# Performance work log

Measured on AMD Instinct MI355X. Metric: run time of the kernel, lower is better.

Reference implementation:

```python
import jax, jax.numpy as jnp
import numpy as np

EPS = 1e-6
K = 20
NUM_OBJECTS = 50
OBJ_FEAT = 256
C_DIM = 128
HIDDEN = 128


def vn_linear(x, W):
    # x: [B, C, 3, ...]; W: [O, C] -> [B, O, 3, ...]
    return jnp.einsum('oc,bc...->bo...', W, x)


def vn_leaky(x, Wdir, slope):
    d = vn_linear(x, Wdir)
    dot = jnp.sum(x * d, axis=2, keepdims=True)
    dsq = jnp.sum(d * d, axis=2, keepdims=True)
    x_neg = x - (dot / (dsq + EPS)) * d
    return slope * x + (1.0 - slope) * jnp.where(dot >= 0, x, x_neg)


def vn_linear_leaky(x, Wfeat, Wdir, slope):
    pf = vn_linear(x, Wfeat)
    d = vn_linear(x, Wdir)
    dot = jnp.sum(pf * d, axis=2, keepdims=True)
    dsq = jnp.sum(d * d, axis=2, keepdims=True)
    p_neg = pf - (dot / (dsq + EPS)) * d
    return slope * pf + (1.0 - slope) * jnp.where(dot >= 0, pf, p_neg)


def resblock(x, fc0, fc1, a0, a1, sc):
    net = vn_linear(vn_leaky(x, a0, 0.0), fc0)
    dx = vn_linear(vn_leaky(net, a1, 0.0), fc1)
    return vn_linear(x, sc) + dx


def get_graph_feature_cross(x, k):
    # x: [B, 3, N] -> edge features [B, 3, 3, N, k]
    inner = -2.0 * jnp.einsum('bdn,bdm->bnm', x, x)
    xx = jnp.sum(x * x, axis=1)                       # [B, N]
    neg_dist = -xx[:, :, None] - inner - xx[:, None, :]  # [B, N, N]
    idx = jax.lax.top_k(neg_dist, k)[1]               # [B, N, k] nearest neighbors
    xt = jnp.transpose(x, (0, 2, 1))                  # [B, N, 3]
    nbr = jax.vmap(lambda pts, ind: pts[ind])(xt, idx)  # [B, N, k, 3]
    ctr = jnp.broadcast_to(xt[:, :, None, :], nbr.shape)
    cross = jnp.cross(nbr, ctr)
    feat = jnp.stack([nbr - ctr, ctr, cross], axis=3)  # [B, N, k, 3, 3]
    return jnp.transpose(feat, (0, 3, 4, 1, 2))


def mlp2(zf, w0, w1, w2):
    h = jax.nn.relu(zf @ w0.T)
    h = jax.nn.relu(h @ w1.T)
    return h @ w2.T


def setup_inputs():
    key = jax.random.key(0)
    ks = jax.random.split(key, 24)
    B, N = 4, 4096

    def rn(k, shape):
        return jax.random.normal(k, shape, dtype=jnp.float32) * (1.0 / np.sqrt(shape[-1]))

    return {
        'p': jax.random.normal(ks[0], (B, N, 3), dtype=jnp.float32),
        'z_idxs': jax.random.randint(ks[1], (B,), 0, NUM_OBJECTS),
        'z': jax.random.normal(ks[2], (NUM_OBJECTS, OBJ_FEAT), dtype=jnp.float32),
        'hw0': rn(ks[3], (OBJ_FEAT, OBJ_FEAT)),
        'hw1': rn(ks[4], (OBJ_FEAT, OBJ_FEAT)),
        'hw2': rn(ks[5], (C_DIM * HIDDEN, OBJ_FEAT)),
        'hb0': rn(ks[6], (OBJ_FEAT, OBJ_FEAT)),
        'hb1': rn(ks[7], (OBJ_FEAT, OBJ_FEAT)),
        'hb2': rn(ks[8], (C_DIM, OBJ_FEAT)),
        'conv_pos_feat': rn(ks[9], (128, 3)),
        'conv_pos_dir': rn(ks[10], (128, 3)),
        'fc_pos_w': rn(ks[11], (2 * HIDDEN, 128)),
        'blk_fc0': rn(ks[12], (5, HIDDEN, 2 * HIDDEN)),
        'blk_fc1': rn(ks[13], (5, HIDDEN, HIDDEN)),
        'blk_act0': rn(ks[14], (5, 2 * HIDDEN, 2 * HIDDEN)),
        'blk_act1': rn(ks[15], (5, HIDDEN, HIDDEN)),
        'blk_sc': rn(ks[16], (5, HIDDEN, 2 * HIDDEN)),
        'actc_dir': rn(ks[17], (HIDDEN, HIDDEN)),
    }


def reference(p, z_idxs, z, hw0, hw1, hw2, hb0, hb1, hb2, conv_pos_feat,
              conv_pos_dir, fc_pos_w, blk_fc0, blk_fc1, blk_act0, blk_act1,
              blk_sc, actc_dir):
    B = p.shape[0]
    x = jnp.transpose(p, (0, 2, 1))                       # [B, 3, N]
    feat = get_graph_feature_cross(x, K)                  # [B, 3, 3, N, k]
    net = vn_linear_leaky(feat, conv_pos_feat, conv_pos_dir, 0.2)  # [B,128,3,N,k]
    net = jnp.mean(net, axis=-1)                          # [B,128,3,N]
    net = vn_linear(net, fc_pos_w)                        # [B,256,3,N]
    for i in range(5):
        net = resblock(net, blk_fc0[i], blk_fc1[i], blk_act0[i], blk_act1[i], blk_sc[i])
        if i < 4:
            pooled = jnp.mean(net, axis=-1, keepdims=True)
            net = jnp.concatenate([net, jnp.broadcast_to(pooled, net.shape)], axis=1)
    net = vn_leaky(jnp.mean(net, axis=-1), actc_dir, 0.2)  # [B, HIDDEN, 3]
    zf = z[z_idxs]                                        # [B, OBJ_FEAT]
    w = mlp2(zf, hw0, hw1, hw2).reshape(B, C_DIM, HIDDEN)  # hypernet weights
    b = mlp2(zf, hb0, hb1, hb2)                           # [B, C_DIM]
    c = jnp.einsum('bhd,bch->bcd', net, w) + b[:, :, None]  # [B, C_DIM, 3]
    return c
```

## Files before the change

kernel.cpp:

```cpp
#include <hip/hip_runtime.h>
#include <hip/hip_fp16.h>
#include <cstdint>
#include <cstddef>

#define NPTS 4096
#define BATCH 4
#define KNN 20

typedef __half f16;
using f32x4 = __attribute__((ext_vector_type(4))) float;
using f16x8 = __attribute__((ext_vector_type(8))) _Float16;

__global__ __launch_bounds__(512) void knn_kernel(const float* __restrict__ p,
                                                  int* __restrict__ idx_out) {
    __shared__ float pts[12288];
    const int tid  = threadIdx.x;
    const int wave = tid >> 6, lane = tid & 63;
    const int b  = blockIdx.x >> 9;
    const int nb = ((blockIdx.x & 511) << 3) + wave;

    const float4* src4 = (const float4*)(p + (size_t)b * NPTS * 3);
    float4* dst4 = (float4*)pts;
    for (int i = tid; i < NPTS * 3 / 4; i += 512) dst4[i] = src4[i];
    __syncthreads();

    const float cx = pts[3 * nb], cy = pts[3 * nb + 1], cz = pts[3 * nb + 2];
    unsigned lst[4];
#pragma unroll
    for (int i = 0; i < 4; i++) lst[i] = 0xFFFFFFFFu;

    for (int t = 0; t < NPTS / 64; t++) {
        int m = (t << 6) + lane;
        float dx = pts[3 * m] - cx, dy = pts[3 * m + 1] - cy, dz = pts[3 * m + 2] - cz;
        float d = dx * dx + dy * dy + dz * dz;
        unsigned c = (__float_as_uint(d) & 0xFFFFF000u) | (unsigned)m;
#pragma unroll
        for (int j = 0; j < 4; j++) {
            unsigned lo = min(c, lst[j]);
            c = max(c, lst[j]);
            lst[j] = lo;
        }
    }

    unsigned lo = 0u, hi = 0xFFFFFFFFu;
    for (int it = 0; it < 32; it++) {
        unsigned mid = lo + ((hi - lo) >> 1);
        int cnt = __popcll(__ballot(lst[0] <= mid)) + __popcll(__ballot(lst[1] <= mid))
                + __popcll(__ballot(lst[2] <= mid)) + __popcll(__ballot(lst[3] <= mid));
        if (cnt >= KNN) hi = mid; else lo = mid + 1;
    }
    const unsigned T = hi;

    unsigned long long bl[4];
#pragma unroll
    for (int j = 0; j < 4; j++) bl[j] = __ballot(lst[j] <= T);
    const unsigned long long lmask = (lane == 63) ? ~0ull >> 1 : (1ull << lane) - 1;
    int base = 0;
    const size_t out_base = ((size_t)b * NPTS + nb) * KNN;
#pragma unroll
    for (int j = 0; j < 4; j++) {
        if (lst[j] <= T) {
            int pos = base + (int)__popcll(bl[j] & lmask);
            idx_out[out_base + pos] = (int)(lst[j] & 0xFFFu);
        }
        base += (int)__popcll(bl[j]);
    }
}

__global__ __launch_bounds__(128) void edgeconv_kernel(
    const float* __restrict__ p, const int* __restrict__ idx,
    const float* __restrict__ wf, const float* __restrict__ wd,
    f16* __restrict__ out) {
    __shared__ float e[KNN][6];
    const int col = blockIdx.x;
    const int b = col >> 12;
    const int tid = threadIdx.x;
    const float cx = p[(size_t)col * 3], cy = p[(size_t)col * 3 + 1], cz = p[(size_t)col * 3 + 2];
    if (tid < KNN) {
        int j = idx[(size_t)col * KNN + tid];
        const float* q = &p[((size_t)b * NPTS + j) * 3];
        float nx = q[0], ny = q[1], nz = q[2];
        e[tid][0] = nx - cx; e[tid][1] = ny - cy; e[tid][2] = nz - cz;
        e[tid][3] = ny * cz - nz * cy;
        e[tid][4] = nz * cx - nx * cz;
        e[tid][5] = nx * cy - ny * cx;
    }
    __syncthreads();
    const int o = tid;
    const float f0 = wf[o * 3], f1 = wf[o * 3 + 1], f2 = wf[o * 3 + 2];
    const float g0 = wd[o * 3], g1 = wd[o * 3 + 1], g2 = wd[o * 3 + 2];
    const float pc0 = f1 * cx, pc1 = f1 * cy, pc2 = f1 * cz;
    const float gc0 = g1 * cx, gc1 = g1 * cy, gc2 = g1 * cz;
    float a0 = 0.f, a1 = 0.f, a2 = 0.f;
    for (int k = 0; k < KNN; k++) {
        float d0 = e[k][0], d1 = e[k][1], d2 = e[k][2];
        float c0 = e[k][3], c1 = e[k][4], c2 = e[k][5];
        float pf0 = fmaf(f0, d0, fmaf(f2, c0, pc0));
        float pf1 = fmaf(f0, d1, fmaf(f2, c1, pc1));
        float pf2 = fmaf(f0, d2, fmaf(f2, c2, pc2));
        float dd0 = fmaf(g0, d0, fmaf(g2, c0, gc0));
        float dd1 = fmaf(g0, d1, fmaf(g2, c1, gc1));
        float dd2 = fmaf(g0, d2, fmaf(g2, c2, gc2));
        float dot = pf0 * dd0 + pf1 * dd1 + pf2 * dd2;
        float dsq = dd0 * dd0 + dd1 * dd1 + dd2 * dd2;
        float w = 0.8f * dot * __builtin_amdgcn_rcpf(dsq + 1e-6f);
        w = (dot >= 0.f) ? 0.f : w;
        a0 += pf0 - w * dd0;
        a1 += pf1 - w * dd1;
        a2 += pf2 - w * dd2;
    }
    const float inv = 1.f / (float)KNN;
    out[((size_t)col * 3 + 0) * 128 + o] = __float2half(a0 * inv);
    out[((size_t)col * 3 + 1) * 128 + o] = __float2half(a1 * inv);
    out[((size_t)col * 3 + 2) * 128 + o] = __float2half(a2 * inv);
}

__global__ __launch_bounds__(128) void compose_kernel(
    const float* __restrict__ act0, const float* __restrict__ scw,
    const float* __restrict__ fcpw, f16* __restrict__ A0F, f16* __restrict__ SCF) {
    const int rowid = blockIdx.x;
    const int c = threadIdx.x;
    if (rowid < 256) {
        float s = 0.f;
        for (int k = 0; k < 256; k++) s += act0[rowid * 256 + k] * fcpw[k * 128 + c];
        A0F[rowid * 128 + c] = __float2half(s);
    } else {
        const int o = rowid - 256;
        float s = 0.f;
        for (int k = 0; k < 256; k++) s += scw[o * 256 + k] * fcpw[k * 128 + c];
        SCF[o * 128 + c] = __float2half(s);
    }
}

template <int KIN>
__global__ __launch_bounds__(256) void resblock_kernel(
    const uint16_t* __restrict__ INg,
    const uint16_t* __restrict__ Wfcp,
    const uint16_t* __restrict__ Wa0,
    const uint16_t* __restrict__ Wfc0,
    const uint16_t* __restrict__ Wa1,
    const uint16_t* __restrict__ Wsc,
    const uint16_t* __restrict__ Wfc1,
    const float* __restrict__ PBg,
    const float* __restrict__ BAg,
    const float* __restrict__ BSCg,
    f16* __restrict__ OUTg,
    float* __restrict__ PPg) {
    constexpr int XRB = 272;
    constexpr int XH_OFF  = (KIN == 256) ? 13056 : 0;
    constexpr int PBS_OFF = 13056;
    constexpr int H0_OFF  = (KIN == 256) ? 26112 : 14592;
    constexpr int MID_OFF = (KIN == 256) ? 13056 : 27648;
    constexpr int LDS_SZ  = (KIN == 256) ? 39168 : 40704;
    __shared__ char lds[LDS_SZ];
    char* INs = lds;
    char* XH  = lds + XH_OFF;
    float* PBs = (float*)(lds + PBS_OFF);
    char* H0h = lds + H0_OFF;
    char* MID = lds + MID_OFF;

    const int tid = threadIdx.x;
    const int lane = tid & 63;
    const int wc = tid >> 6;
    const int gr0 = blockIdx.x * 48;
    const int b = blockIdx.x >> 8;

    if (KIN == 128) {
        for (int i = tid; i < 384; i += 256) PBs[i] = PBg[b * 384 + i];
    }
    {
#pragma unroll
        for (int j = 0; j < 3; j++) {
            int chunk = tid + j * 256;
            int row = chunk >> 4, c16 = chunk & 15;
            f16x8 v = *(const f16x8*)(INg + (size_t)(gr0 + row) * 128 + c16 * 8);
            *(f16x8*)(INs + row * 272 + c16 * 16) = v;
        }
    }
    __syncthreads();

    f32x4 midAcc[3][2];
#pragma unroll
    for (int i = 0; i < 3; i++) { midAcc[i][0] = (f32x4){0,0,0,0}; midAcc[i][1] = (f32x4){0,0,0,0}; }

#pragma unroll
    for (int half = 0; half < 2; half++) {
        {
            f32x4 acc[3][2];
#pragma unroll
            for (int i = 0; i < 3; i++) { acc[i][0] = (f32x4){0,0,0,0}; acc[i][1] = (f32x4){0,0,0,0}; }
#pragma unroll
            for (int ks = 0; ks < 4; ks++) {
                const int kb = ks * 64 + (lane >> 4) * 16;
                f16x8 af[3], bf[2];
#pragma unroll
                for (int mi = 0; mi < 3; mi++) {
                    int r = mi * 16 + (lane & 15);
                    af[mi] = *(const f16x8*)(INs + r * 272 + kb);
                }
#pragma unroll
                for (int ni = 0; ni < 2; ni++) {
                    int o = half * 128 + wc * 32 + ni * 16 + (lane & 15);
                    if (KIN == 256)
                        bf[ni] = *(const f16x8*)(Wa0 + o * 128 + ks * 32 + (lane >> 4) * 8);
                    else
                        bf[ni] = *(const f16x8*)(Wa0 + o * 256 + ks * 32 + (lane >> 4) * 8);
                }
#pragma unroll
                for (int mi = 0; mi < 3; mi++)
#pragma unroll
                    for (int ni = 0; ni < 2; ni++)
                        acc[mi][ni] = __builtin_amdgcn_mfma_f32_16x16x32_f16(
                            af[mi], bf[ni], acc[mi][ni], 0, 0, 0);
            }
#pragma unroll
            for (int mi = 0; mi < 3; mi++)
#pragma unroll
                for (int ni = 0; ni < 2; ni++) {
                    int col = wc * 32 + ni * 16 + (lane & 15);
#pragma unroll
                    for (int r = 0; r < 4; r++) {
                        int row = mi * 16 + (lane >> 4) * 4 + r;
                        float v = acc[mi][ni][r];
                        if (KIN == 128)
                            v += BAg[b * 768 + (row % 3) * 256 + half * 128 + col];
                        *(f16*)(H0h + row * 272 + col * 2) = __float2half(v);
                    }
                }
        }
        if (KIN == 256) {
            f32x4 acc[3][2];
#pragma unroll
            for (int i = 0; i < 3; i++) { acc[i][0] = (f32x4){0,0,0,0}; acc[i][1] = (f32x4){0,0,0,0}; }
#pragma unroll
            for (int ks = 0; ks < 4; ks++) {
                const int kb = ks * 64 + (lane >> 4) * 16;
                f16x8 af[3], bf[2];
#pragma unroll
                for (int mi = 0; mi < 3; mi++) {
                    int r = mi * 16 + (lane & 15);
                    af[mi] = *(const f16x8*)(INs + r * 272 + kb);
                }
#pragma unroll
                for (int ni = 0; ni < 2; ni++) {
                    int o = half * 128 + wc * 32 + ni * 16 + (lane & 15);
                    bf[ni] = *(const f16x8*)(Wfcp + o * 128 + ks * 32 + (lane >> 4) * 8);
                }
#pragma unroll
                for (int mi = 0; mi < 3; mi++)
#pragma unroll
                    for (int ni = 0; ni < 2; ni++)
                        acc[mi][ni] = __builtin_amdgcn_mfma_f32_16x16x32_f16(
                            af[mi], bf[ni], acc[mi][ni], 0, 0, 0);
            }
#pragma unroll
            for (int mi = 0; mi < 3; mi++)
#pragma unroll
                for (int ni = 0; ni < 2; ni++) {
                    int col = wc * 32 + ni * 16 + (lane & 15);
#pragma unroll
                    for (int r = 0; r < 4; r++) {
                        int row = mi * 16 + (lane >> 4) * 4 + r;
                        *(f16*)(XH + row * 272 + col * 2) = __float2half(acc[mi][ni][r]);
                    }
                }
        }
        __syncthreads();
#pragma unroll
        for (int j = 0; j < 4; j++) {
            int it = tid + j * 256;
            int pnt = it >> 6, cp = it & 63;
            float xv[3][2], dv[3][2];
#pragma unroll
            for (int s = 0; s < 3; s++) {
                int row = pnt * 3 + s;
                __half2 d2 = *(const __half2*)(H0h + row * 272 + cp * 4);
                dv[s][0] = __half2float(d2.x); dv[s][1] = __half2float(d2.y);
                if (KIN == 256) {
                    __half2 x2 = *(const __half2*)(XH + row * 272 + cp * 4);
                    xv[s][0] = __half2float(x2.x); xv[s][1] = __half2float(x2.y);
                } else {
                    if (half == 0) {
                        __half2 x2 = *(const __half2*)(INs + row * 272 + cp * 4);
                        xv[s][0] = __half2float(x2.x); xv[s][1] = __half2float(x2.y);
                    } else {
                        xv[s][0] = PBs[s * 128 + cp * 2];
                        xv[s][1] = PBs[s * 128 + cp * 2 + 1];
                    }
                }
            }
#pragma unroll
            for (int jj = 0; jj < 2; jj++) {
                float dot = xv[0][jj] * dv[0][jj] + xv[1][jj] * dv[1][jj] + xv[2][jj] * dv[2][jj];
                float dsq = dv[0][jj] * dv[0][jj] + dv[1][jj] * dv[1][jj] + dv[2][jj] * dv[2][jj];
                float coef = dot * __builtin_amdgcn_rcpf(dsq + 1e-6f);
                bool pos = dot >= 0.f;
#pragma unroll
                for (int s = 0; s < 3; s++)
                    xv[s][jj] = pos ? xv[s][jj] : xv[s][jj] - coef * dv[s][jj];
            }
#pragma unroll
            for (int s = 0; s < 3; s++) {
                int row = pnt * 3 + s;
                __half2 h2;
                h2.x = __float2half(xv[s][0]);
                h2.y = __float2half(xv[s][1]);
                *(__half2*)(H0h + row * 272 + cp * 4) = h2;
            }
        }
        __syncthreads();
#pragma unroll
        for (int ks = 0; ks < 4; ks++) {
            const int kb = ks * 64 + (lane >> 4) * 16;
            f16x8 af[3], bf[2];
#pragma unroll
            for (int mi = 0; mi < 3; mi++) {
                int r = mi * 16 + (lane & 15);
                af[mi] = *(const f16x8*)(H0h + r * 272 + kb);
            }
#pragma unroll
            for (int ni = 0; ni < 2; ni++) {
                int o = wc * 32 + ni * 16 + (lane & 15);
                bf[ni] = *(const f16x8*)(Wfc0 + o * 256 + half * 128 + ks * 32 + (lane >> 4) * 8);
            }
#pragma unroll
            for (int mi = 0; mi < 3; mi++)
#pragma unroll
                for (int ni = 0; ni < 2; ni++)
                    midAcc[mi][ni] = __builtin_amdgcn_mfma_f32_16x16x32_f16(
                        af[mi], bf[ni], midAcc[mi][ni], 0, 0, 0);
        }
        __syncthreads();
    }

#pragma unroll
    for (int mi = 0; mi < 3; mi++)
#pragma unroll
        for (int ni = 0; ni < 2; ni++) {
            int col = wc * 32 + ni * 16 + (lane & 15);
#pragma unroll
            for (int r = 0; r < 4; r++) {
                int row = mi * 16 + (lane >> 4) * 4 + r;
                *(f16*)(MID + row * 272 + col * 2) = __float2half(midAcc[mi][ni][r]);
            }
        }
    __syncthreads();

    {
        f32x4 acc[3][2];
#pragma unroll
        for (int i = 0; i < 3; i++) { acc[i][0] = (f32x4){0,0,0,0}; acc[i][1] = (f32x4){0,0,0,0}; }
#pragma unroll
        for (int ks = 0; ks < 4; ks++) {
            const int kb = ks * 64 + (lane >> 4) * 16;
            f16x8 af[3], bf[2];
#pragma unroll
            for (int mi = 0; mi < 3; mi++) {
                int r = mi * 16 + (lane & 15);
                af[mi] = *(const f16x8*)(MID + r * 272 + kb);
            }
#pragma unroll
            for (int ni = 0; ni < 2; ni++) {
                int o = wc * 32 + ni * 16 + (lane & 15);
                bf[ni] = *(const f16x8*)(Wa1 + o * 128 + ks * 32 + (lane >> 4) * 8);
            }
#pragma unroll
            for (int mi = 0; mi < 3; mi++)
#pragma unroll
                for (int ni = 0; ni < 2; ni++)
                    acc[mi][ni] = __builtin_amdgcn_mfma_f32_16x16x32_f16(
                        af[mi], bf[ni], acc[mi][ni], 0, 0, 0);
        }
#pragma unroll
        for (int mi = 0; mi < 3; mi++)
#pragma unroll
            for (int ni = 0; ni < 2; ni++) {
                int col = wc * 32 + ni * 16 + (lane & 15);
#pragma unroll
                for (int r = 0; r < 4; r++) {
                    int row = mi * 16 + (lane >> 4) * 4 + r;
                    *(f16*)(H0h + row * 272 + col * 2) = __float2half(acc[mi][ni][r]);
                }
            }
    }
    __syncthreads();
#pragma unroll
    for (int j = 0; j < 4; j++) {
        int it = tid + j * 256;
        int pnt = it >> 6, cp = it & 63;
        float xv[3][2], dv[3][2];
#pragma unroll
        for (int s = 0; s < 3; s++) {
            int row = pnt * 3 + s;
            __half2 d2 = *(const __half2*)(H0h + row * 272 + cp * 4);
            __half2 x2 = *(const __half2*)(MID + row * 272 + cp * 4);
            dv[s][0] = __half2float(d2.x); dv[s][1] = __half2float(d2.y);
            xv[s][0] = __half2float(x2.x); xv[s][1] = __half2float(x2.y);
        }
#pragma unroll
        for (int jj = 0; jj < 2; jj++) {
            float dot = xv[0][jj] * dv[0][jj] + xv[1][jj] * dv[1][jj] + xv[2][jj] * dv[2][jj];
            float dsq = dv[0][jj] * dv[0][jj] + dv[1][jj] * dv[1][jj] + dv[2][jj] * dv[2][jj];
            float coef = dot * __builtin_amdgcn_rcpf(dsq + 1e-6f);
            bool pos = dot >= 0.f;
#pragma unroll
            for (int s = 0; s < 3; s++)
                xv[s][jj] = pos ? xv[s][jj] : xv[s][jj] - coef * dv[s][jj];
        }
#pragma unroll
        for (int s = 0; s < 3; s++) {
            int row = pnt * 3 + s;
            __half2 h2;
            h2.x = __float2half(xv[s][0]);
            h2.y = __float2half(xv[s][1]);
            *(__half2*)(H0h + row * 272 + cp * 4) = h2;
        }
    }
    __syncthreads();

    {
        f32x4 acc[3][2];
#pragma unroll
        for (int i = 0; i < 3; i++) { acc[i][0] = (f32x4){0,0,0,0}; acc[i][1] = (f32x4){0,0,0,0}; }
#pragma unroll
        for (int ks = 0; ks < 8; ks++) {
            const int kelem = ks * 32;
            f16x8 af[3], bf[2];
            if (kelem < 128) {
                const int kb = kelem * 2 + (lane >> 4) * 16;
#pragma unroll
                for (int mi = 0; mi < 3; mi++) {
                    int r = mi * 16 + (lane & 15);
                    af[mi] = *(const f16x8*)(INs + r * 272 + kb);
                }
#pragma unroll
                for (int ni = 0; ni < 2; ni++) {
                    int o = wc * 32 + ni * 16 + (lane & 15);
                    if (KIN == 256)
                        bf[ni] = *(const f16x8*)(Wsc + o * 128 + kelem + (lane >> 4) * 8);
                    else
                        bf[ni] = *(const f16x8*)(Wsc + o * 256 + kelem + (lane >> 4) * 8);
                }
            } else {
                const int kk = kelem - 128;
                const int kb = kk * 2 + (lane >> 4) * 16;
#pragma unroll
                for (int mi = 0; mi < 3; mi++) {
                    int r = mi * 16 + (lane & 15);
                    af[mi] = *(const f16x8*)(H0h + r * 272 + kb);
                }
#pragma unroll
                for (int ni = 0; ni < 2; ni++) {
                    int o = wc * 32 + ni * 16 + (lane & 15);
                    bf[ni] = *(const f16x8*)(Wfc1 + o * 128 + kk + (lane >> 4) * 8);
                }
            }
#pragma unroll
            for (int mi = 0; mi < 3; mi++)
#pragma unroll
                for (int ni = 0; ni < 2; ni++)
                    acc[mi][ni] = __builtin_amdgcn_mfma_f32_16x16x32_f16(
                        af[mi], bf[ni], acc[mi][ni], 0, 0, 0);
        }
        float ps[2][3] = {};
#pragma unroll
        for (int mi = 0; mi < 3; mi++)
#pragma unroll
            for (int ni = 0; ni < 2; ni++) {
                int col = wc * 32 + ni * 16 + (lane & 15);
#pragma unroll
                for (int r = 0; r < 4; r++) {
                    int row = mi * 16 + (lane >> 4) * 4 + r;
                    float v = acc[mi][ni][r];
                    if (KIN == 128) v += BSCg[b * 384 + (row % 3) * 128 + col];
                    OUTg[(size_t)(gr0 + row) * 128 + col] = __float2half(v);
                    ps[ni][row % 3] += v;
                }
            }
#pragma unroll
        for (int ni = 0; ni < 2; ni++)
#pragma unroll
            for (int s = 0; s < 3; s++) {
                float x = ps[ni][s];
                x += __shfl_xor(x, 16, 64);
                x += __shfl_xor(x, 32, 64);
                ps[ni][s] = x;
            }
        if ((lane >> 4) == 0) {
#pragma unroll
            for (int ni = 0; ni < 2; ni++) {
                int col = wc * 32 + ni * 16 + (lane & 15);
#pragma unroll
                for (int s = 0; s < 3; s++)
                    PPg[(size_t)blockIdx.x * 384 + s * 128 + col] = ps[ni][s];
            }
        }
    }
}

__global__ __launch_bounds__(512) void poolbias_kernel(
    const float* __restrict__ PP, const f16* __restrict__ a0n, const f16* __restrict__ scn,
    float* __restrict__ PB, float* __restrict__ BA, float* __restrict__ BSC, int hasbias) {
    __shared__ float red[4][128];
    __shared__ float pl[128];
    const int bs = blockIdx.x;
    const int b = bs / 3, s = bs % 3;
    const int t = threadIdx.x;
    const int col = t & 127, seg = t >> 7;
    {
        float acc = 0.f;
        const float* base = PP + (size_t)(b * 256) * 384 + s * 128 + col;
        for (int k = seg * 64; k < seg * 64 + 64; k++) acc += base[(size_t)k * 384];
        red[seg][col] = acc;
    }
    __syncthreads();
    if (t < 128) {
        float a = (red[0][t] + red[1][t]) + (red[2][t] + red[3][t]);
        a *= (1.f / (float)NPTS);
        pl[t] = a;
        PB[bs * 128 + t] = a;
    }
    __syncthreads();
    if (!hasbias) return;
    if (t < 256) {
        float s2 = 0.f;
        for (int c = 0; c < 128; c++) s2 += __half2float(a0n[t * 256 + 128 + c]) * pl[c];
        BA[bs * 256 + t] = s2;
    } else if (t < 384) {
        int o = t - 256;
        float s2 = 0.f;
        for (int c = 0; c < 128; c++) s2 += __half2float(scn[o * 256 + 128 + c]) * pl[c];
        BSC[bs * 128 + o] = s2;
    }
}

__global__ void cvt_all(const float* __restrict__ fcpw, const float* __restrict__ act0,
                        const float* __restrict__ fc0, const float* __restrict__ act1,
                        const float* __restrict__ fc1, const float* __restrict__ scw,
                        f16* o_fcpw, f16* o_act0, f16* o_fc0, f16* o_act1, f16* o_fc1,
                        f16* o_scw) {
    int i = blockIdx.x * 256 + threadIdx.x;
    if (i < 32768) { o_fcpw[i] = __float2half(fcpw[i]); }
    else if (i < 360448) { int j = i - 32768;  o_act0[j] = __float2half(act0[j]); }
    else if (i < 524288) { int j = i - 360448; o_fc0[j]  = __float2half(fc0[j]); }
    else if (i < 606208) { int j = i - 524288; o_act1[j] = __float2half(act1[j]); }
    else if (i < 688128) { int j = i - 606208; o_fc1[j]  = __float2half(fc1[j]); }
    else                 { int j = i - 688128; o_scw[j]  = __float2half(scw[j]); }
}

__global__ __launch_bounds__(256) void hypermlp_kernel(
    const float* __restrict__ z, const int* __restrict__ zidx,
    const float* __restrict__ hw0, const float* __restrict__ hw1,
    const float* __restrict__ hb0, const float* __restrict__ hb1,
    const float* __restrict__ hb2,
    float* __restrict__ H2, float* __restrict__ BV) {
    __shared__ float zf[256], ta[256], tb[256];
    const int b = blockIdx.x, o = threadIdx.x;
    zf[o] = z[(size_t)zidx[b] * 256 + o];
    __syncthreads();
    float s = 0.f;
    for (int c = 0; c < 256; c++) s += zf[c] * hw0[o * 256 + c];
    ta[o] = fmaxf(s, 0.f);
    __syncthreads();
    s = 0.f;
    for (int c = 0; c < 256; c++) s += ta[c] * hw1[o * 256 + c];
    tb[o] = fmaxf(s, 0.f);
    __syncthreads();
    H2[(size_t)b * 256 + o] = tb[o];
    s = 0.f;
    for (int c = 0; c < 256; c++) s += zf[c] * hb0[o * 256 + c];
    __syncthreads();
    ta[o] = fmaxf(s, 0.f);
    __syncthreads();
    s = 0.f;
    for (int c = 0; c < 256; c++) s += ta[c] * hb1[o * 256 + c];
    __syncthreads();
    tb[o] = fmaxf(s, 0.f);
    __syncthreads();
    if (o < 128) {
        s = 0.f;
        for (int c = 0; c < 256; c++) s += tb[c] * hb2[o * 256 + c];
        BV[(size_t)b * 128 + o] = s;
    }
}

__global__ __launch_bounds__(256) void wmat_kernel(const float* __restrict__ H2,
                                                   const float* __restrict__ hw2,
                                                   float* __restrict__ WM) {
    __shared__ float h[256];
    const int b = blockIdx.y;
    const int row = blockIdx.x * 256 + threadIdx.x;
    h[threadIdx.x] = H2[(size_t)b * 256 + threadIdx.x];
    __syncthreads();
    float s = 0.f;
    for (int c = 0; c < 256; c++) s += h[c] * hw2[(size_t)row * 256 + c];
    WM[(size_t)b * 16384 + row] = s;
}

__global__ __launch_bounds__(384) void final_out_kernel(
    const float* __restrict__ pb, const float* __restrict__ actc,
    const float* __restrict__ WM, const float* __restrict__ BV,
    float* __restrict__ out) {
    __shared__ float pb2s[3][128];
    const int b = blockIdx.x;
    const int t = threadIdx.x;
    if (t < 128) {
        const int o = t;
        float d0 = 0.f, d1 = 0.f, d2 = 0.f;
        for (int c = 0; c < 128; c++) {
            float w = actc[o * 128 + c];
            d0 += w * pb[(size_t)(b * 3 + 0) * 128 + c];
            d1 += w * pb[(size_t)(b * 3 + 1) * 128 + c];
            d2 += w * pb[(size_t)(b * 3 + 2) * 128 + c];
        }
        float x0 = pb[(size_t)(b * 3 + 0) * 128 + o];
        float x1 = pb[(size_t)(b * 3 + 1) * 128 + o];
        float x2 = pb[(size_t)(b * 3 + 2) * 128 + o];
        float dot = x0 * d0 + x1 * d1 + x2 * d2;
        float dsq = d0 * d0 + d1 * d1 + d2 * d2;
        float coef = dot / (dsq + 1e-6f);
        bool pos = dot >= 0.f;
        float h0 = pos ? x0 : x0 - coef * d0;
        float h1 = pos ? x1 : x1 - coef * d1;
        float h2 = pos ? x2 : x2 - coef * d2;
        pb2s[0][o] = 0.2f * x0 + 0.8f * h0;
        pb2s[1][o] = 0.2f * x1 + 0.8f * h1;
        pb2s[2][o] = 0.2f * x2 + 0.8f * h2;
    }
    __syncthreads();
    const int cd = t / 3, d = t % 3;
    float s = BV[(size_t)b * 128 + cd];
    for (int h = 0; h < 128; h++)
        s += pb2s[d][h] * WM[(size_t)b * 16384 + cd * 128 + h];
    out[(size_t)b * 384 + cd * 3 + d] = s;
}

extern "C" void kernel_launch(void* const* d_in, const int* in_sizes, int n_in,
                              void* d_out, int out_size, void* d_ws, size_t ws_size,
                              hipStream_t stream) {
    (void)in_sizes; (void)n_in; (void)out_size; (void)ws_size;
    const float* p     = (const float*)d_in[0];
    const int*   zidx  = (const int*)d_in[1];
    const float* z     = (const float*)d_in[2];
    const float* hw0   = (const float*)d_in[3];
    const float* hw1   = (const float*)d_in[4];
    const float* hw2   = (const float*)d_in[5];
    const float* hb0   = (const float*)d_in[6];
    const float* hb1   = (const float*)d_in[7];
    const float* hb2   = (const float*)d_in[8];
    const float* cpf   = (const float*)d_in[9];
    const float* cpd   = (const float*)d_in[10];
    const float* fcpw  = (const float*)d_in[11];
    const float* fc0w  = (const float*)d_in[12];
    const float* fc1w  = (const float*)d_in[13];
    const float* act0  = (const float*)d_in[14];
    const float* act1  = (const float*)d_in[15];
    const float* scw   = (const float*)d_in[16];
    const float* actc  = (const float*)d_in[17];
    float* out = (float*)d_out;
    char* ws = (char*)d_ws;

    int*   IDX   = (int*)(ws + 0);
    f16*   MB    = (f16*)(ws + 1310720);
    f16*   MB2   = (f16*)(ws + 13893632);
    f16*   FCPW16= (f16*)(ws + 26476544);
    f16*   ACT0W = (f16*)(ws + 26542080);
    f16*   FC0W  = (f16*)(ws + 27197440);
    f16*   ACT1W = (f16*)(ws + 27525120);
    f16*   FC1W  = (f16*)(ws + 27688960);
    f16*   SCW16 = (f16*)(ws + 27852800);
    float* PP    = (float*)(ws + 28180480);
    float* PB    = (float*)(ws + 29753344);
    float* H2    = (float*)(ws + 29759488);
    float* BV    = (float*)(ws + 29763584);
    float* WM    = (float*)(ws + 29765632);
    float* BA    = (float*)(ws + 30027776);
    float* BSC   = (float*)(ws + 30040064);
    f16*   A0F   = (f16*)(ws + 30046208);
    f16*   SCF   = (f16*)(ws + 30111744);

    cvt_all<<<3328, 256, 0, stream>>>(fcpw, act0, fc0w, act1, fc1w, scw,
                                      FCPW16, ACT0W, FC0W, ACT1W, FC1W, SCW16);
    compose_kernel<<<384, 128, 0, stream>>>(act0, scw, fcpw, A0F, SCF);

    knn_kernel<<<BATCH * NPTS / 8, 512, 0, stream>>>(p, IDX);
    edgeconv_kernel<<<BATCH * NPTS, 128, 0, stream>>>(p, IDX, cpf, cpd, MB);

    resblock_kernel<256><<<1024, 256, 0, stream>>>(
        (const uint16_t*)MB, (const uint16_t*)FCPW16,
        (const uint16_t*)A0F, (const uint16_t*)FC0W,
        (const uint16_t*)ACT1W, (const uint16_t*)SCF, (const uint16_t*)FC1W,
        nullptr, nullptr, nullptr, MB2, PP);
    poolbias_kernel<<<12, 512, 0, stream>>>(PP, ACT0W + 1 * 65536, SCW16 + 1 * 32768,
                                            PB, BA, BSC, 1);

    for (int i = 1; i < 5; i++) {
        const f16* a0h = ACT0W + (size_t)i * 256 * 256;
        const f16* sch = SCW16 + (size_t)i * 128 * 256;
        f16* in  = (i & 1) ? MB2 : MB;
        f16* ob  = (i & 1) ? MB : MB2;
        resblock_kernel<128><<<1024, 256, 0, stream>>>(
            (const uint16_t*)in, nullptr,
            (const uint16_t*)a0h,
            (const uint16_t*)(FC0W + (size_t)i * 128 * 256),
            (const uint16_t*)(ACT1W + (size_t)i * 128 * 128),
            (const uint16_t*)sch,
            (const uint16_t*)(FC1W + (size_t)i * 128 * 128),
            PB, BA, BSC, ob, PP);
        if (i < 4) {
            poolbias_kernel<<<12, 512, 0, stream>>>(
                PP, ACT0W + (size_t)(i + 1) * 65536, SCW16 + (size_t)(i + 1) * 32768,
                PB, BA, BSC, 1);
        } else {
            poolbias_kernel<<<12, 512, 0, stream>>>(PP, nullptr, nullptr, PB, BA, BSC, 0);
        }
    }

    hypermlp_kernel<<<4, 256, 0, stream>>>(z, zidx, hw0, hw1, hb0, hb1, hb2, H2, BV);
    wmat_kernel<<<dim3(64, 4), 256, 0, stream>>>(H2, hw2, WM);
    final_out_kernel<<<4, 384, 0, stream>>>(PB, actc, WM, BV, out);
}
```

Measured before the change: 379.9 us.

## Transpose hypernet weights for coalesced MLP reads and batch wmat across batches

Adds a kernel that transposes the hypernetwork weight matrices so each thread reads them with a coalesced column pattern. The MLP kernel is split into two blocks per batch, one for the weight path and one for the bias path, so the two run in parallel. The wmat kernel now reads each hw2 row once with wave-level reductions and reuses it for all four batches instead of once per batch. The cost is an extra transpose launch and extra workspace, and the hypernet tail is a small part of total time.

```diff
diff --git a/kernel.cpp b/kernel.cpp
--- a/kernel.cpp
+++ b/kernel.cpp
@@ -132,6 +132,18 @@
     }
 }
 
+__global__ void transpose_hyper(const float* __restrict__ hw0, const float* __restrict__ hw1,
+                                const float* __restrict__ hb0, const float* __restrict__ hb1,
+                                const float* __restrict__ hb2,
+                                float* T0, float* T1, float* T2, float* T3, float* T4) {
+    int i = blockIdx.x * 256 + threadIdx.x;
+    if (i < 65536)        T0[(i & 255) * 256 + (i >> 8)] = hw0[i];
+    else if (i < 131072)  { int j = i - 65536;  T1[(j & 255) * 256 + (j >> 8)] = hw1[j]; }
+    else if (i < 196608)  { int j = i - 131072; T2[(j & 255) * 256 + (j >> 8)] = hb0[j]; }
+    else if (i < 262144)  { int j = i - 196608; T3[(j & 255) * 256 + (j >> 8)] = hb1[j]; }
+    else if (i < 294912)  { int j = i - 262144; T4[(j & 255) * 128 + (j >> 8)] = hb2[j]; }
+}
+
 template <int KIN>
 __global__ __launch_bounds__(256) void resblock_kernel(
     const uint16_t* __restrict__ INg,
@@ -146,7 +158,6 @@
     const float* __restrict__ BSCg,
     f16* __restrict__ OUTg,
     float* __restrict__ PPg) {
-    constexpr int XRB = 272;
     constexpr int XH_OFF  = (KIN == 256) ? 13056 : 0;
     constexpr int PBS_OFF = 13056;
     constexpr int H0_OFF  = (KIN == 256) ? 26112 : 14592;
@@ -548,53 +559,72 @@
     else                 { int j = i - 688128; o_scw[j]  = __float2half(scw[j]); }
 }
 
-__global__ __launch_bounds__(256) void hypermlp_kernel(
+__global__ __launch_bounds__(256) void hypermlp2_kernel(
     const float* __restrict__ z, const int* __restrict__ zidx,
-    const float* __restrict__ hw0, const float* __restrict__ hw1,
-    const float* __restrict__ hb0, const float* __restrict__ hb1,
-    const float* __restrict__ hb2,
+    const float* __restrict__ T0, const float* __restrict__ T1,
+    const float* __restrict__ T2, const float* __restrict__ T3,
+    const float* __restrict__ T4,
     float* __restrict__ H2, float* __restrict__ BV) {
     __shared__ float zf[256], ta[256], tb[256];
-    const int b = blockIdx.x, o = threadIdx.x;
+    const int b = blockIdx.x, path = blockIdx.y, o = threadIdx.x;
     zf[o] = z[(size_t)zidx[b] * 256 + o];
     __syncthreads();
-    float s = 0.f;
-    for (int c = 0; c < 256; c++) s += zf[c] * hw0[o * 256 + c];
-    ta[o] = fmaxf(s, 0.f);
-    __syncthreads();
-    s = 0.f;
-    for (int c = 0; c < 256; c++) s += ta[c] * hw1[o * 256 + c];
-    tb[o] = fmaxf(s, 0.f);
-    __syncthreads();
-    H2[(size_t)b * 256 + o] = tb[o];
-    s = 0.f;
-    for (int c = 0; c < 256; c++) s += zf[c] * hb0[o * 256 + c];
-    __syncthreads();
-    ta[o] = fmaxf(s, 0.f);
-    __syncthreads();
-    s = 0.f;
-    for (int c = 0; c < 256; c++) s += ta[c] * hb1[o * 256 + c];
-    __syncthreads();
-    tb[o] = fmaxf(s, 0.f);
-    __syncthreads();
-    if (o < 128) {
+    if (path == 0) {
+        float s = 0.f;
+        for (int c = 0; c < 256; c++) s += zf[c] * T0[c * 256 + o];
+        ta[o] = fmaxf(s, 0.f);
+        __syncthreads();
         s = 0.f;
-        for (int c = 0; c < 256; c++) s += tb[c] * hb2[o * 256 + c];
-        BV[(size_t)b * 128 + o] = s;
-    }
-}
-
-__global__ __launch_bounds__(256) void wmat_kernel(const float* __restrict__ H2,
-                                                   const float* __restrict__ hw2,
-                                                   float* __restrict__ WM) {
-    __shared__ float h[256];
-    const int b = blockIdx.y;
-    const int row = blockIdx.x * 256 + threadIdx.x;
-    h[threadIdx.x] = H2[(size_t)b * 256 + threadIdx.x];
-    __syncthreads();
-    float s = 0.f;
-    for (int c = 0; c < 256; c++) s += h[c] * hw2[(size_t)row * 256 + c];
-    WM[(size_t)b * 16384 + row] = s;
+        for (int c = 0; c < 256; c++) s += ta[c] * T1[c * 256 + o];
+        H2[(size_t)b * 256 + o] = fmaxf(s, 0.f);
+    } else {
+        float s = 0.f;
+        for (int c = 0; c < 256; c++) s += zf[c] * T2[c * 256 + o];
+        ta[o] = fmaxf(s, 0.f);
+        __syncthreads();
+        s = 0.f;
+        for (int c = 0; c < 256; c++) s += ta[c] * T3[c * 256 + o];
+        tb[o] = fmaxf(s, 0.f);
+        __syncthreads();
+        if (o < 128) {
+            s = 0.f;
+            for (int c = 0; c < 256; c++) s += tb[c] * T4[c * 128 + o];
+            BV[(size_t)b * 128 + o] = s;
+        }
+    }
+}
+
+__global__ __launch_bounds__(256) void wmat2_kernel(const float* __restrict__ H2,
+                                                    const float* __restrict__ hw2,
+                                                    float* __restrict__ WM) {
+    __shared__ float h[4][256];
+    const int t = threadIdx.x;
+    for (int i = t; i < 1024; i += 256) h[i >> 8][i & 255] = H2[i];
+    __syncthreads();
+    const int wave = t >> 6, lane = t & 63;
+    for (int r = 0; r < 16; r++) {
+        int row = blockIdx.x * 64 + wave * 16 + r;
+        float s0 = 0.f, s1 = 0.f, s2 = 0.f, s3 = 0.f;
+#pragma unroll
+        for (int q = 0; q < 4; q++) {
+            int c = q * 64 + lane;
+            float w = hw2[(size_t)row * 256 + c];
+            s0 += h[0][c] * w; s1 += h[1][c] * w; s2 += h[2][c] * w; s3 += h[3][c] * w;
+        }
+#pragma unroll
+        for (int off = 32; off > 0; off >>= 1) {
+            s0 += __shfl_xor(s0, off, 64);
+            s1 += __shfl_xor(s1, off, 64);
+            s2 += __shfl_xor(s2, off, 64);
+            s3 += __shfl_xor(s3, off, 64);
+        }
+        if (lane == 0) {
+            WM[(size_t)0 * 16384 + row] = s0;
+            WM[(size_t)1 * 16384 + row] = s1;
+            WM[(size_t)2 * 16384 + row] = s2;
+            WM[(size_t)3 * 16384 + row] = s3;
+        }
+    }
 }
 
 __global__ __launch_bounds__(384) void final_out_kernel(
@@ -678,10 +708,16 @@
     float* BSC   = (float*)(ws + 30040064);
     f16*   A0F   = (f16*)(ws + 30046208);
     f16*   SCF   = (f16*)(ws + 30111744);
+    float* T0    = (float*)(ws + 30144512);
+    float* T1    = (float*)(ws + 30406656);
+    float* T2    = (float*)(ws + 30668800);
+    float* T3    = (float*)(ws + 30930944);
+    float* T4    = (float*)(ws + 31193088);
 
     cvt_all<<<3328, 256, 0, stream>>>(fcpw, act0, fc0w, act1, fc1w, scw,
                                       FCPW16, ACT0W, FC0W, ACT1W, FC1W, SCW16);
     compose_kernel<<<384, 128, 0, stream>>>(act0, scw, fcpw, A0F, SCF);
+    transpose_hyper<<<1152, 256, 0, stream>>>(hw0, hw1, hb0, hb1, hb2, T0, T1, T2, T3, T4);
 
     knn_kernel<<<BATCH * NPTS / 8, 512, 0, stream>>>(p, IDX);
     edgeconv_kernel<<<BATCH * NPTS, 128, 0, stream>>>(p, IDX, cpf, cpd, MB);
@@ -716,7 +752,7 @@
         }
     }
 
-    hypermlp_kernel<<<4, 256, 0, stream>>>(z, zidx, hw0, hw1, hb0, hb1, hb2, H2, BV);
-    wmat_kernel<<<dim3(64, 4), 256, 0, stream>>>(H2, hw2, WM);
+    hypermlp2_kernel<<<dim3(4, 2), 256, 0, stream>>>(z, zidx, T0, T1, T2, T3, T4, H2, BV);
+    wmat2_kernel<<<256, 256, 0, stream>>>(H2, hw2, WM);
     final_out_kernel<<<4, 384, 0, stream>>>(PB, actc, WM, BV, out);
 }
```

Result: faster. 371.2 us (-2.3%).
